# Kernel optimization log

Measured on AMD Instinct MI355X. Metric: run time of the kernel, lower is better.

Reference implementation:

```python
import jax, jax.numpy as jnp
import numpy as np

BN_EPS = 1e-5
NUM_GC_LAYERS = 3
NUM_LAYERS = NUM_GC_LAYERS + 4  # 7
N_NODES = 50000
N_EDGES = 600000
DIM = 128


def setup_inputs() -> dict:
    key = jax.random.key(0)
    ks = jax.random.split(key, 9)
    x = jax.random.normal(ks[0], (N_NODES, DIM), dtype=jnp.float32)
    edge_index = jax.random.randint(ks[1], (2, N_EDGES), 0, N_NODES, dtype=jnp.int64)
    batch = jnp.zeros((N_NODES,), dtype=jnp.int64)
    s = 0.1
    W1 = jax.random.normal(ks[2], (NUM_LAYERS, DIM, DIM), dtype=jnp.float32) * s
    b1 = jax.random.normal(ks[3], (NUM_LAYERS, DIM), dtype=jnp.float32) * s
    W2 = jax.random.normal(ks[4], (NUM_LAYERS, DIM, DIM), dtype=jnp.float32) * s
    b2 = jax.random.normal(ks[5], (NUM_LAYERS, DIM), dtype=jnp.float32) * s
    gamma = jnp.ones((NUM_LAYERS, DIM), dtype=jnp.float32)
    beta = jnp.zeros((NUM_LAYERS, DIM), dtype=jnp.float32)
    return {"x": x, "edge_index": edge_index, "batch": batch,
            "W1": W1, "b1": b1, "W2": W2, "b2": b2,
            "gamma": gamma, "beta": beta}


def _gin_conv(x, src, dst, W1, b1, W2, b2):
    # GINConv with eps=0: out = MLP(x + sum_{j in N(i)} x_j)
    agg = jax.ops.segment_sum(x[src], dst, num_segments=x.shape[0])  # [N, D]
    h = x + agg
    h = jnp.maximum(h @ W1 + b1, 0.0) @ W2 + b2
    return h


def _batch_norm(h, g, b):
    # BatchNorm1d in training mode: biased batch stats over nodes
    mean = jnp.mean(h, axis=0)
    var = jnp.var(h, axis=0)
    return (h - mean) * jax.lax.rsqrt(var + BN_EPS) * g + b


def reference(x, edge_index, batch, W1, b1, W2, b2, gamma, beta):
    src, dst = edge_index[0], edge_index[1]
    for i in range(NUM_GC_LAYERS):
        h = _gin_conv(x, src, dst, W1[i], b1[i], W2[i], b2[i])
        x = _batch_norm(jnp.maximum(h, 0.0), gamma[i], beta[i])
    j = NUM_GC_LAYERS
    outs = []
    for k in range(j, j + 4):
        h = _gin_conv(x, src, dst, W1[k], b1[k], W2[k], b2[k])
        outs.append(_batch_norm(jnp.tanh(h), gamma[k], beta[k]))
    return tuple(outs)
```

## Files before the change

kernel.cpp:

```cpp
#include <hip/hip_runtime.h>
#include <math.h>

#define NN 50000
#define NE 600000
#define DIM 128
#define NLAYERS 7
#define LDK 136
#define BN_EPS 1e-5f
#define GB 782
#define PART_SLOT 200192

typedef __attribute__((ext_vector_type(4))) float floatx4;
typedef __attribute__((ext_vector_type(8))) _Float16 half8;
typedef __attribute__((ext_vector_type(2))) _Float16 half2v;

__device__ __forceinline__ unsigned short f2h(float f) {
  _Float16 h = (_Float16)f;
  return __builtin_bit_cast(unsigned short, h);
}
__device__ __forceinline__ float2 up(unsigned int u) {
  half2v h = __builtin_bit_cast(half2v, u);
  return make_float2((float)h.x, (float)h.y);
}
__device__ __forceinline__ unsigned int pk(float a, float b) {
  half2v h;
  h.x = (_Float16)a;
  h.y = (_Float16)b;
  return __builtin_bit_cast(unsigned int, h);
}


__global__ void hist_kernel(const int* __restrict__ ei, int* __restrict__ deg) {
  int e = blockIdx.x * 256 + threadIdx.x;
  if (e < NE) atomicAdd(&deg[ei[NE + e]], 1);
}

__global__ __launch_bounds__(256) void scan_part(const int* __restrict__ deg,
                                                 int* __restrict__ rowl,
                                                 int* __restrict__ bsum) {
  int b = blockIdx.x, t = threadIdx.x;
  int base = b * 1024 + t * 4;
  int d[4];
  #pragma unroll
  for (int j = 0; j < 4; j++) d[j] = (base + j < NN) ? deg[base + j] : 0;
  int s = d[0] + d[1] + d[2] + d[3];
  int lane = t & 63;
  int incl = s;
  #pragma unroll
  for (int off = 1; off < 64; off <<= 1) {
    int n = __shfl_up(incl, off);
    if (lane >= off) incl += n;
  }
  __shared__ int wtot[4];
  if (lane == 63) wtot[t >> 6] = incl;
  __syncthreads();
  int woff = 0;
  for (int w = 0; w < (t >> 6); w++) woff += wtot[w];
  int run = woff + incl - s;
  #pragma unroll
  for (int j = 0; j < 4; j++) {
    if (base + j < NN) rowl[base + j] = run;
    run += d[j];
  }
  if (t == 255) bsum[b] = woff + incl;
}

__global__ void scan_top(const int* __restrict__ bsum, int* __restrict__ boff,
                         int* __restrict__ row) {
  int t = threadIdx.x;
  int v = (t < 49) ? bsum[t] : 0;
  int incl = v;
  #pragma unroll
  for (int off = 1; off < 64; off <<= 1) {
    int n = __shfl_up(incl, off);
    if (t >= off) incl += n;
  }
  if (t < 49) boff[t] = incl - v;
  if (t == 48) row[NN] = incl;
}

__global__ __launch_bounds__(256) void scan_apply(const int* __restrict__ rowl,
                                                  const int* __restrict__ boff,
                                                  int* __restrict__ row,
                                                  int* __restrict__ cur) {
  int i = blockIdx.x * 256 + threadIdx.x;
  if (i < NN) {
    int r = rowl[i] + boff[i >> 10];
    row[i] = r;
    cur[i] = r;
  }
}

__global__ void bucket_kernel(const int* __restrict__ ei, int* __restrict__ cur,
                              int* __restrict__ esrc) {
  int e = blockIdx.x * 256 + threadIdx.x;
  if (e < NE) {
    int d = ei[NE + e];
    int p = atomicAdd(&cur[d], 1);
    esrc[p] = ei[e];
  }
}


__global__ void convw_kernel(const float* __restrict__ W1, const float* __restrict__ W2,
                             unsigned short* __restrict__ wb) {
  int i = blockIdx.x * 256 + threadIdx.x;
  if (i >= NLAYERS * 16384) return;
  int l = i >> 14;
  int r = i & 16383;
  int n = r >> 7;
  int k = r & 127;
  wb[(size_t)(l * 2 + 0) * 16384 + n * 128 + k] = f2h(W1[(size_t)l * 16384 + k * 128 + n]);
  wb[(size_t)(l * 2 + 1) * 16384 + n * 128 + k] = f2h(W2[(size_t)l * 16384 + k * 128 + n]);
}

__global__ __launch_bounds__(256) void convx_kernel(const float* __restrict__ x,
                                                    unsigned int* __restrict__ x16) {
  int i = blockIdx.x * 256 + threadIdx.x;
  float4 v = ((const float4*)x)[i];
  uint2 o;
  o.x = pk(v.x, v.y);
  o.y = pk(v.z, v.w);
  ((uint2*)x16)[i] = o;
}


__global__ __launch_bounds__(256) void gather_kernel(
    const unsigned int* __restrict__ x16, const int* __restrict__ esrc,
    const int* __restrict__ row, unsigned int* __restrict__ agg16) {
  int w = (blockIdx.x * 256 + threadIdx.x) >> 6;
  int lane = threadIdx.x & 63;
  if (w >= NN) return;
  int s0 = row[w], s1 = row[w + 1];
  float ax = 0.f, ay = 0.f;
  int e = s0;
  for (; e + 3 < s1; e += 4) {
    int i0 = esrc[e], i1 = esrc[e + 1], i2 = esrc[e + 2], i3 = esrc[e + 3];
    unsigned int v0 = x16[i0 * 64 + lane];
    unsigned int v1 = x16[i1 * 64 + lane];
    unsigned int v2 = x16[i2 * 64 + lane];
    unsigned int v3 = x16[i3 * 64 + lane];
    float2 f0 = up(v0), f1 = up(v1), f2 = up(v2), f3 = up(v3);
    ax += (f0.x + f1.x) + (f2.x + f3.x);
    ay += (f0.y + f1.y) + (f2.y + f3.y);
  }
  for (; e < s1; e++) {
    float2 f = up(x16[esrc[e] * 64 + lane]);
    ax += f.x;
    ay += f.y;
  }
  agg16[w * 64 + lane] = pk(ax, ay);
}


__global__ __launch_bounds__(256) void mlp1_kernel(
    const unsigned int* __restrict__ x16, const unsigned int* __restrict__ agg16,
    const unsigned short* __restrict__ wb,
    const float* __restrict__ b1, const float* __restrict__ b2,
    unsigned short* __restrict__ xout16, float* __restrict__ part,
    const float* __restrict__ bnPrev, const float* __restrict__ gPrev,
    const float* __restrict__ btPrev, const int* __restrict__ deg, int hasPrev) {
  __shared__ unsigned short hS[64 * LDK];
  __shared__ unsigned short wS[128 * LDK];
  __shared__ float scshS[256];
  int tid = threadIdx.x;
  int row0 = blockIdx.x * 64;

  if (tid < 128) {
    float sc = 1.f, sh = 0.f;
    if (hasPrev) {
      const float inv = 1.f / (float)NN;
      float mean = bnPrev[tid] * inv;
      float var = bnPrev[128 + tid] * inv - mean * mean;
      sc = gPrev[tid] * rsqrtf(var + BN_EPS);
      sh = btPrev[tid] - mean * sc;
    }
    scshS[tid] = sc;
    scshS[128 + tid] = sh;
  }
  __syncthreads();

  for (int idx = tid; idx < 1024; idx += 256) {
    int r = idx >> 4;
    int c = (idx & 15) * 8;
    uint4 hv = {0u, 0u, 0u, 0u};
    if (row0 + r < NN) {
      size_t base = (size_t)(row0 + r) * 16 + (c >> 3);
      uint4 xv = ((const uint4*)x16)[base];
      uint4 av = ((const uint4*)agg16)[base];
      float dr = 1.f + (float)deg[row0 + r];
      unsigned int xs[4] = {xv.x, xv.y, xv.z, xv.w};
      unsigned int as_[4] = {av.x, av.y, av.z, av.w};
      unsigned int hs[4];
      #pragma unroll
      for (int j = 0; j < 4; j++) {
        float2 xf = up(xs[j]);
        float2 af = up(as_[j]);
        int cc = c + j * 2;
        float h0 = scshS[cc] * (xf.x + af.x) + dr * scshS[128 + cc];
        float h1 = scshS[cc + 1] * (xf.y + af.y) + dr * scshS[128 + cc + 1];
        hs[j] = pk(h0, h1);
      }
      hv.x = hs[0]; hv.y = hs[1]; hv.z = hs[2]; hv.w = hs[3];
    }
    *(uint4*)&hS[r * LDK + c] = hv;
  }
  for (int q = tid; q < 2048; q += 256) {
    int rw = q >> 4;
    int c8 = (q & 15) * 8;
    *(uint4*)&wS[rw * LDK + c8] = *(const uint4*)(wb + rw * 128 + c8);
  }
  __syncthreads();

  int lane = tid & 63;
  int wav = tid >> 6;
  int quad = lane >> 4;
  int lm = lane & 15;
  int mrow = wav * 16 + lm;

  floatx4 acc[8];
  #pragma unroll
  for (int nt = 0; nt < 8; nt++) {
    floatx4 c = {0.f, 0.f, 0.f, 0.f};
    #pragma unroll
    for (int ks = 0; ks < 4; ks++) {
      half8 af = *(half8*)&hS[mrow * LDK + ks * 32 + quad * 8];
      half8 bf = *(half8*)&wS[(nt * 16 + lm) * LDK + ks * 32 + quad * 8];
      c = __builtin_amdgcn_mfma_f32_16x16x32_f16(af, bf, c, 0, 0, 0);
    }
    acc[nt] = c;
  }
  #pragma unroll
  for (int nt = 0; nt < 8; nt++) {
    float bv = b1[nt * 16 + lm];
    #pragma unroll
    for (int rg = 0; rg < 4; rg++) {
      float v = acc[nt][rg] + bv;
      v = v > 0.f ? v : 0.f;
      hS[(wav * 16 + quad * 4 + rg) * LDK + nt * 16 + lm] = f2h(v);
    }
  }
  __syncthreads();
  for (int q = tid; q < 2048; q += 256) {
    int rw = q >> 4;
    int c8 = (q & 15) * 8;
    *(uint4*)&wS[rw * LDK + c8] = *(const uint4*)(wb + 16384 + rw * 128 + c8);
  }
  __syncthreads();

  bool wvalid = (row0 + wav * 16) < NN;
  float sArr[8], sqArr[8];
  #pragma unroll
  for (int nt = 0; nt < 8; nt++) {
    floatx4 c = {0.f, 0.f, 0.f, 0.f};
    #pragma unroll
    for (int ks = 0; ks < 4; ks++) {
      half8 af = *(half8*)&hS[mrow * LDK + ks * 32 + quad * 8];
      half8 bf = *(half8*)&wS[(nt * 16 + lm) * LDK + ks * 32 + quad * 8];
      c = __builtin_amdgcn_mfma_f32_16x16x32_f16(af, bf, c, 0, 0, 0);
    }
    float bv = b2[nt * 16 + lm];
    float s = 0.f, sq = 0.f;
    #pragma unroll
    for (int rg = 0; rg < 4; rg++) {
      float v = c[rg] + bv;
      v = v > 0.f ? v : 0.f;
      if (wvalid)
        xout16[(size_t)(row0 + wav * 16 + quad * 4 + rg) * DIM + nt * 16 + lm] = f2h(v);
      s += v;
      sq += v * v;
    }
    s += __shfl_xor(s, 16);
    s += __shfl_xor(s, 32);
    sq += __shfl_xor(sq, 16);
    sq += __shfl_xor(sq, 32);
    sArr[nt] = s;
    sqArr[nt] = sq;
  }
  __syncthreads();
  float* redS = (float*)hS;
  if (quad == 0) {
    #pragma unroll
    for (int nt = 0; nt < 8; nt++) {
      redS[wav * 256 + nt * 16 + lm] = wvalid ? sArr[nt] : 0.f;
      redS[wav * 256 + 128 + nt * 16 + lm] = wvalid ? sqArr[nt] : 0.f;
    }
  }
  __syncthreads();
  float v = redS[tid] + redS[256 + tid] + redS[512 + tid] + redS[768 + tid];
  part[(size_t)blockIdx.x * 256 + tid] = v;
}


__global__ __launch_bounds__(256) void mlp4_kernel(
    const unsigned int* __restrict__ x16, const unsigned int* __restrict__ agg16,
    const unsigned short* __restrict__ wbg,
    const float* __restrict__ b1g, const float* __restrict__ b2g,
    float* __restrict__ out, float* __restrict__ partBase,
    const float* __restrict__ bnPrev, const float* __restrict__ gPrev,
    const float* __restrict__ btPrev, const int* __restrict__ deg) {
  __shared__ unsigned short hS[64 * LDK];
  __shared__ unsigned short wS[128 * LDK];
  __shared__ float scshS[256];
  int tid = threadIdx.x;
  int row0 = blockIdx.x * 64;

  if (tid < 128) {
    const float inv = 1.f / (float)NN;
    float mean = bnPrev[tid] * inv;
    float var = bnPrev[128 + tid] * inv - mean * mean;
    float sc = gPrev[tid] * rsqrtf(var + BN_EPS);
    scshS[tid] = sc;
    scshS[128 + tid] = btPrev[tid] - mean * sc;
  }
  __syncthreads();

  for (int idx = tid; idx < 1024; idx += 256) {
    int r = idx >> 4;
    int c = (idx & 15) * 8;
    uint4 hv = {0u, 0u, 0u, 0u};
    if (row0 + r < NN) {
      size_t base = (size_t)(row0 + r) * 16 + (c >> 3);
      uint4 xv = ((const uint4*)x16)[base];
      uint4 av = ((const uint4*)agg16)[base];
      float dr = 1.f + (float)deg[row0 + r];
      unsigned int xs[4] = {xv.x, xv.y, xv.z, xv.w};
      unsigned int as_[4] = {av.x, av.y, av.z, av.w};
      unsigned int hs[4];
      #pragma unroll
      for (int j = 0; j < 4; j++) {
        float2 xf = up(xs[j]);
        float2 af = up(as_[j]);
        int cc = c + j * 2;
        float h0 = scshS[cc] * (xf.x + af.x) + dr * scshS[128 + cc];
        float h1 = scshS[cc + 1] * (xf.y + af.y) + dr * scshS[128 + cc + 1];
        hs[j] = pk(h0, h1);
      }
      hv.x = hs[0]; hv.y = hs[1]; hv.z = hs[2]; hv.w = hs[3];
    }
    *(uint4*)&hS[r * LDK + c] = hv;
  }
  __syncthreads();

  int lane = tid & 63;
  int wav = tid >> 6;
  int quad = lane >> 4;
  int lm = lane & 15;
  int mrow = wav * 16 + lm;
  bool wvalid = (row0 + wav * 16) < NN;

  half8 aF[4];
  #pragma unroll
  for (int ks = 0; ks < 4; ks++)
    aF[ks] = *(half8*)&hS[mrow * LDK + ks * 32 + quad * 8];

  #pragma unroll 1
  for (int ly = 0; ly < 4; ly++) {
    int layer = 3 + ly;
    const unsigned short* wb = wbg + (size_t)layer * 2 * 16384;
    const float* b1 = b1g + layer * 128;
    const float* b2 = b2g + layer * 128;
    float* act = out + (size_t)ly * NN * DIM;
    float* part = partBase + (size_t)ly * PART_SLOT;

    __syncthreads();
    for (int q = tid; q < 2048; q += 256) {
      int rw = q >> 4;
      int c8 = (q & 15) * 8;
      *(uint4*)&wS[rw * LDK + c8] = *(const uint4*)(wb + rw * 128 + c8);
    }
    __syncthreads();

    floatx4 acc[8];
    #pragma unroll
    for (int nt = 0; nt < 8; nt++) {
      floatx4 c = {0.f, 0.f, 0.f, 0.f};
      #pragma unroll
      for (int ks = 0; ks < 4; ks++) {
        half8 bf = *(half8*)&wS[(nt * 16 + lm) * LDK + ks * 32 + quad * 8];
        c = __builtin_amdgcn_mfma_f32_16x16x32_f16(aF[ks], bf, c, 0, 0, 0);
      }
      acc[nt] = c;
    }
    #pragma unroll
    for (int nt = 0; nt < 8; nt++) {
      float bv = b1[nt * 16 + lm];
      #pragma unroll
      for (int rg = 0; rg < 4; rg++) {
        float v = acc[nt][rg] + bv;
        v = v > 0.f ? v : 0.f;
        hS[(wav * 16 + quad * 4 + rg) * LDK + nt * 16 + lm] = f2h(v);
      }
    }
    __syncthreads();
    for (int q = tid; q < 2048; q += 256) {
      int rw = q >> 4;
      int c8 = (q & 15) * 8;
      *(uint4*)&wS[rw * LDK + c8] = *(const uint4*)(wb + 16384 + rw * 128 + c8);
    }
    __syncthreads();

    float sArr[8], sqArr[8];
    #pragma unroll
    for (int nt = 0; nt < 8; nt++) {
      floatx4 c = {0.f, 0.f, 0.f, 0.f};
      #pragma unroll
      for (int ks = 0; ks < 4; ks++) {
        half8 af = *(half8*)&hS[mrow * LDK + ks * 32 + quad * 8];
        half8 bf = *(half8*)&wS[(nt * 16 + lm) * LDK + ks * 32 + quad * 8];
        c = __builtin_amdgcn_mfma_f32_16x16x32_f16(af, bf, c, 0, 0, 0);
      }
      float bv = b2[nt * 16 + lm];
      float s = 0.f, sq = 0.f;
      #pragma unroll
      for (int rg = 0; rg < 4; rg++) {
        float v = c[rg] + bv;
        v = tanhf(v);
        if (wvalid)
          act[(size_t)(row0 + wav * 16 + quad * 4 + rg) * DIM + nt * 16 + lm] = v;
        s += v;
        sq += v * v;
      }
      s += __shfl_xor(s, 16);
      s += __shfl_xor(s, 32);
      sq += __shfl_xor(sq, 16);
      sq += __shfl_xor(sq, 32);
      sArr[nt] = s;
      sqArr[nt] = sq;
    }
    __syncthreads();
    float* redS = (float*)hS;
    if (quad == 0) {
      #pragma unroll
      for (int nt = 0; nt < 8; nt++) {
        redS[wav * 256 + nt * 16 + lm] = wvalid ? sArr[nt] : 0.f;
        redS[wav * 256 + 128 + nt * 16 + lm] = wvalid ? sqArr[nt] : 0.f;
      }
    }
    __syncthreads();
    float v = redS[tid] + redS[256 + tid] + redS[512 + tid] + redS[768 + tid];
    part[(size_t)blockIdx.x * 256 + tid] = v;
  }
}


__global__ __launch_bounds__(256) void reduce_kernel(const float* __restrict__ part,
                                                     float* __restrict__ bn) {
  int c = blockIdx.x;
  int t = threadIdx.x;
  const float* p = part + (size_t)blockIdx.y * PART_SLOT + c;
  float s = 0.f;
  for (int b = t; b < GB; b += 256) s += p[(size_t)b * 256];
  #pragma unroll
  for (int off = 1; off < 64; off <<= 1) s += __shfl_xor(s, off);
  __shared__ float wsum[4];
  if ((t & 63) == 0) wsum[t >> 6] = s;
  __syncthreads();
  if (t == 0) bn[blockIdx.y * 256 + c] = wsum[0] + wsum[1] + wsum[2] + wsum[3];
}


__global__ __launch_bounds__(256) void norm_kernel(
    const float* __restrict__ aBase, const float* __restrict__ bnAll,
    const float* __restrict__ gammaAll, const float* __restrict__ betaAll,
    float* __restrict__ oBase, int layer0) {
  int layer = layer0 + blockIdx.y;
  const float* a = aBase + (size_t)blockIdx.y * NN * DIM;
  const float* bn = bnAll + blockIdx.y * 256;
  const float* gamma = gammaAll + layer * 128;
  const float* beta = betaAll + layer * 128;
  float* o = oBase + (size_t)blockIdx.y * NN * DIM;
  int i = blockIdx.x * 256 + threadIdx.x;
  int f = (i & 31) * 4;
  const float inv = 1.f / (float)NN;
  float4 v = ((const float4*)a)[i];
  float r[4] = {v.x, v.y, v.z, v.w};
  #pragma unroll
  for (int j = 0; j < 4; j++) {
    float mean = bn[f + j] * inv;
    float var = bn[128 + f + j] * inv - mean * mean;
    float sc = gamma[f + j] * rsqrtf(var + BN_EPS);
    r[j] = (r[j] - mean) * sc + beta[f + j];
  }
  float4 ov; ov.x = r[0]; ov.y = r[1]; ov.z = r[2]; ov.w = r[3];
  ((float4*)o)[i] = ov;
}


extern "C" void kernel_launch(void* const* d_in, const int* in_sizes, int n_in,
                              void* d_out, int out_size, void* d_ws, size_t ws_size,
                              hipStream_t stream) {
  const float* x_in = (const float*)d_in[0];
  const int* ei = (const int*)d_in[1];
  const float* W1g = (const float*)d_in[3];
  const float* b1g = (const float*)d_in[4];
  const float* W2g = (const float*)d_in[5];
  const float* b2g = (const float*)d_in[6];
  const float* gg = (const float*)d_in[7];
  const float* bg = (const float*)d_in[8];
  float* out = (float*)d_out;

  char* ws = (char*)d_ws;
  const size_t OFF_X16 = 0;
  const size_t OFF_A16 = 12800000;
  const size_t OFF_WB = 25600000;
  const size_t OFF_BN = 26058752;
  const size_t OFF_DEG = 26062848;
  const size_t OFF_ROW = 26262848;
  const size_t OFF_CUR = 26462852;
  const size_t OFF_ESR = 26662852;
  const size_t OFF_PART = 29062852;

  unsigned int* X16 = (unsigned int*)(ws + OFF_X16);
  unsigned int* A16 = (unsigned int*)(ws + OFF_A16);
  unsigned short* wb = (unsigned short*)(ws + OFF_WB);
  float* bn = (float*)(ws + OFF_BN);
  int* deg = (int*)(ws + OFF_DEG);
  int* rowp = (int*)(ws + OFF_ROW);
  int* cur = (int*)(ws + OFF_CUR);
  int* esrc = (int*)(ws + OFF_ESR);
  float* part = (float*)(ws + OFF_PART);
  int* rowl = (int*)(ws + OFF_PART);
  int* bsum = (int*)(ws + OFF_PART + 800000);
  int* boff = (int*)(ws + OFF_PART + 800256);

  hipMemsetAsync(deg, 0, NN * sizeof(int), stream);
  hist_kernel<<<(NE + 255) / 256, 256, 0, stream>>>(ei, deg);
  scan_part<<<49, 256, 0, stream>>>(deg, rowl, bsum);
  scan_top<<<1, 64, 0, stream>>>(bsum, boff, rowp);
  scan_apply<<<196, 256, 0, stream>>>(rowl, boff, rowp, cur);
  bucket_kernel<<<(NE + 255) / 256, 256, 0, stream>>>(ei, cur, esrc);
  convw_kernel<<<(NLAYERS * 16384 + 255) / 256, 256, 0, stream>>>(W1g, W2g, wb);
  convx_kernel<<<NN * DIM / 4 / 256, 256, 0, stream>>>(x_in, X16);

  for (int i = 0; i < 3; i++) {
    gather_kernel<<<(NN * 64 + 255) / 256, 256, 0, stream>>>(X16, esrc, rowp, A16);
    mlp1_kernel<<<GB, 256, 0, stream>>>(
        X16, A16, wb + (size_t)i * 2 * 16384, b1g + i * 128, b2g + i * 128,
        (unsigned short*)X16, part,
        (i == 0) ? bn : bn + (i - 1) * 256,
        (i == 0) ? gg : gg + (i - 1) * 128,
        (i == 0) ? bg : bg + (i - 1) * 128, deg, i > 0 ? 1 : 0);
    reduce_kernel<<<dim3(256, 1), 256, 0, stream>>>(part, bn + i * 256);
  }
  gather_kernel<<<(NN * 64 + 255) / 256, 256, 0, stream>>>(X16, esrc, rowp, A16);
  mlp4_kernel<<<GB, 256, 0, stream>>>(X16, A16, wb, b1g, b2g, out, part,
                                      bn + 2 * 256, gg + 2 * 128, bg + 2 * 128, deg);
  reduce_kernel<<<dim3(256, 4), 256, 0, stream>>>(part, bn);
  norm_kernel<<<dim3(NN * DIM / 4 / 256, 4), 256, 0, stream>>>(out, bn, gg, bg, out, 3);
}
```

Measured before the change: 519.1 us.

## Halve MLP shared memory with XOR swizzle and register-prefetched weight halves

The MLP kernels drop the padded LDS layout for an XOR-swizzled 128-wide one and stage weights in 64-row halves, so each block uses about half the shared memory and launch bounds request four blocks per CU. The next weight half is prefetched into registers while MFMAs run on the current one, and biases are folded into the accumulator init. The tanh layers use an exp/rcp fast tanh, and the gather loop is unrolled by eight to keep more loads in flight. The cost is extra barriers per layer, more register pressure, and slightly less accurate tanh.

```diff
diff --git a/kernel.cpp b/kernel.cpp
--- a/kernel.cpp
+++ b/kernel.cpp
@@ -5,7 +5,6 @@
 #define NE 600000
 #define DIM 128
 #define NLAYERS 7
-#define LDK 136
 #define BN_EPS 1e-5f
 #define GB 782
 #define PART_SLOT 200192
@@ -27,6 +26,13 @@
   h.x = (_Float16)a;
   h.y = (_Float16)b;
   return __builtin_bit_cast(unsigned int, h);
+}
+__device__ __forceinline__ float tanh_fast(float x) {
+  float e = __expf(2.0f * x);
+  return 1.0f - 2.0f * __builtin_amdgcn_rcpf(e + 1.0f);
+}
+__device__ __forceinline__ int hsw(int row, int scol) {
+  return row * 128 + (scol ^ ((row & 7) << 3));
 }
 
 
@@ -134,6 +140,20 @@
   int s0 = row[w], s1 = row[w + 1];
   float ax = 0.f, ay = 0.f;
   int e = s0;
+  for (; e + 7 < s1; e += 8) {
+    int idx[8];
+    #pragma unroll
+    for (int j = 0; j < 8; j++) idx[j] = esrc[e + j];
+    unsigned int v[8];
+    #pragma unroll
+    for (int j = 0; j < 8; j++) v[j] = x16[idx[j] * 64 + lane];
+    #pragma unroll
+    for (int j = 0; j < 8; j++) {
+      float2 f = up(v[j]);
+      ax += f.x;
+      ay += f.y;
+    }
+  }
   for (; e + 3 < s1; e += 4) {
     int i0 = esrc[e], i1 = esrc[e + 1], i2 = esrc[e + 2], i3 = esrc[e + 3];
     unsigned int v0 = x16[i0 * 64 + lane];
@@ -153,15 +173,15 @@
 }
 
 
-__global__ __launch_bounds__(256) void mlp1_kernel(
+__global__ __launch_bounds__(256, 4) void mlp1_kernel(
     const unsigned int* __restrict__ x16, const unsigned int* __restrict__ agg16,
     const unsigned short* __restrict__ wb,
     const float* __restrict__ b1, const float* __restrict__ b2,
     unsigned short* __restrict__ xout16, float* __restrict__ part,
     const float* __restrict__ bnPrev, const float* __restrict__ gPrev,
     const float* __restrict__ btPrev, const int* __restrict__ deg, int hasPrev) {
-  __shared__ unsigned short hS[64 * LDK];
-  __shared__ unsigned short wS[128 * LDK];
+  __shared__ unsigned short hS[64 * 128];
+  __shared__ unsigned short wS[64 * 128];
   __shared__ float scshS[256];
   int tid = threadIdx.x;
   int row0 = blockIdx.x * 64;
@@ -178,37 +198,41 @@
     scshS[tid] = sc;
     scshS[128 + tid] = sh;
   }
-  __syncthreads();
-
-  for (int idx = tid; idx < 1024; idx += 256) {
+
+  uint4 wreg[4];
+  #pragma unroll
+  for (int j = 0; j < 4; j++) {
+    int q = tid + j * 256;
+    wreg[j] = *(const uint4*)(wb + (q >> 4) * 128 + (q & 15) * 8);
+  }
+  __syncthreads();
+
+  #pragma unroll
+  for (int j = 0; j < 4; j++) {
+    int idx = tid + j * 256;
     int r = idx >> 4;
     int c = (idx & 15) * 8;
     uint4 hv = {0u, 0u, 0u, 0u};
     if (row0 + r < NN) {
-      size_t base = (size_t)(row0 + r) * 16 + (c >> 3);
+      size_t base = (size_t)(row0 + r) * 16 + (idx & 15);
       uint4 xv = ((const uint4*)x16)[base];
       uint4 av = ((const uint4*)agg16)[base];
       float dr = 1.f + (float)deg[row0 + r];
       unsigned int xs[4] = {xv.x, xv.y, xv.z, xv.w};
       unsigned int as_[4] = {av.x, av.y, av.z, av.w};
-      unsigned int hs[4];
-      #pragma unroll
-      for (int j = 0; j < 4; j++) {
-        float2 xf = up(xs[j]);
-        float2 af = up(as_[j]);
-        int cc = c + j * 2;
+      unsigned int hs4[4];
+      #pragma unroll
+      for (int jj = 0; jj < 4; jj++) {
+        float2 xf = up(xs[jj]);
+        float2 af = up(as_[jj]);
+        int cc = c + jj * 2;
         float h0 = scshS[cc] * (xf.x + af.x) + dr * scshS[128 + cc];
         float h1 = scshS[cc + 1] * (xf.y + af.y) + dr * scshS[128 + cc + 1];
-        hs[j] = pk(h0, h1);
-      }
-      hv.x = hs[0]; hv.y = hs[1]; hv.z = hs[2]; hv.w = hs[3];
-    }
-    *(uint4*)&hS[r * LDK + c] = hv;
-  }
-  for (int q = tid; q < 2048; q += 256) {
-    int rw = q >> 4;
-    int c8 = (q & 15) * 8;
-    *(uint4*)&wS[rw * LDK + c8] = *(const uint4*)(wb + rw * 128 + c8);
+        hs4[jj] = pk(h0, h1);
+      }
+      hv.x = hs4[0]; hv.y = hs4[1]; hv.z = hs4[2]; hv.w = hs4[3];
+    }
+    *(uint4*)&hS[hsw(r, c)] = hv;
   }
   __syncthreads();
 
@@ -217,53 +241,122 @@
   int quad = lane >> 4;
   int lm = lane & 15;
   int mrow = wav * 16 + lm;
+  bool wvalid = (row0 + wav * 16) < NN;
+
+  half8 aF[4];
+  #pragma unroll
+  for (int ks = 0; ks < 4; ks++)
+    aF[ks] = *(half8*)&hS[hsw(mrow, ks * 32 + quad * 8)];
+
+  #pragma unroll
+  for (int j = 0; j < 4; j++) {
+    int q = tid + j * 256;
+    *(uint4*)&wS[hsw(q >> 4, (q & 15) * 8)] = wreg[j];
+  }
+  #pragma unroll
+  for (int j = 0; j < 4; j++) {
+    int q = tid + j * 256;
+    wreg[j] = *(const uint4*)(wb + 8192 + (q >> 4) * 128 + (q & 15) * 8);
+  }
+  __syncthreads();
 
   floatx4 acc[8];
   #pragma unroll
+  for (int nt = 0; nt < 4; nt++) {
+    float bv = b1[nt * 16 + lm];
+    floatx4 cacc = {bv, bv, bv, bv};
+    #pragma unroll
+    for (int ks = 0; ks < 4; ks++) {
+      half8 bf = *(half8*)&wS[hsw(nt * 16 + lm, ks * 32 + quad * 8)];
+      cacc = __builtin_amdgcn_mfma_f32_16x16x32_f16(aF[ks], bf, cacc, 0, 0, 0);
+    }
+    acc[nt] = cacc;
+  }
+  __syncthreads();
+  #pragma unroll
+  for (int j = 0; j < 4; j++) {
+    int q = tid + j * 256;
+    *(uint4*)&wS[hsw(q >> 4, (q & 15) * 8)] = wreg[j];
+  }
+  #pragma unroll
+  for (int j = 0; j < 4; j++) {
+    int q = tid + j * 256;
+    wreg[j] = *(const uint4*)(wb + 16384 + (q >> 4) * 128 + (q & 15) * 8);
+  }
+  __syncthreads();
+  #pragma unroll
+  for (int nt = 4; nt < 8; nt++) {
+    float bv = b1[nt * 16 + lm];
+    floatx4 cacc = {bv, bv, bv, bv};
+    #pragma unroll
+    for (int ks = 0; ks < 4; ks++) {
+      half8 bf = *(half8*)&wS[hsw((nt - 4) * 16 + lm, ks * 32 + quad * 8)];
+      cacc = __builtin_amdgcn_mfma_f32_16x16x32_f16(aF[ks], bf, cacc, 0, 0, 0);
+    }
+    acc[nt] = cacc;
+  }
+  #pragma unroll
   for (int nt = 0; nt < 8; nt++) {
-    floatx4 c = {0.f, 0.f, 0.f, 0.f};
+    #pragma unroll
+    for (int rg = 0; rg < 4; rg++) {
+      float v = acc[nt][rg];
+      v = v > 0.f ? v : 0.f;
+      hS[hsw(wav * 16 + quad * 4 + rg, nt * 16 + lm)] = f2h(v);
+    }
+  }
+  __syncthreads();
+  #pragma unroll
+  for (int j = 0; j < 4; j++) {
+    int q = tid + j * 256;
+    *(uint4*)&wS[hsw(q >> 4, (q & 15) * 8)] = wreg[j];
+  }
+  #pragma unroll
+  for (int j = 0; j < 4; j++) {
+    int q = tid + j * 256;
+    wreg[j] = *(const uint4*)(wb + 24576 + (q >> 4) * 128 + (q & 15) * 8);
+  }
+  __syncthreads();
+  half8 aG[4];
+  #pragma unroll
+  for (int ks = 0; ks < 4; ks++)
+    aG[ks] = *(half8*)&hS[hsw(mrow, ks * 32 + quad * 8)];
+  #pragma unroll
+  for (int nt = 0; nt < 4; nt++) {
+    float bv = b2[nt * 16 + lm];
+    floatx4 cacc = {bv, bv, bv, bv};
     #pragma unroll
     for (int ks = 0; ks < 4; ks++) {
-      half8 af = *(half8*)&hS[mrow * LDK + ks * 32 + quad * 8];
-      half8 bf = *(half8*)&wS[(nt * 16 + lm) * LDK + ks * 32 + quad * 8];
-      c = __builtin_amdgcn_mfma_f32_16x16x32_f16(af, bf, c, 0, 0, 0);
-    }
-    acc[nt] = c;
-  }
+      half8 bf = *(half8*)&wS[hsw(nt * 16 + lm, ks * 32 + quad * 8)];
+      cacc = __builtin_amdgcn_mfma_f32_16x16x32_f16(aG[ks], bf, cacc, 0, 0, 0);
+    }
+    acc[nt] = cacc;
+  }
+  __syncthreads();
+  #pragma unroll
+  for (int j = 0; j < 4; j++) {
+    int q = tid + j * 256;
+    *(uint4*)&wS[hsw(q >> 4, (q & 15) * 8)] = wreg[j];
+  }
+  __syncthreads();
+  #pragma unroll
+  for (int nt = 4; nt < 8; nt++) {
+    float bv = b2[nt * 16 + lm];
+    floatx4 cacc = {bv, bv, bv, bv};
+    #pragma unroll
+    for (int ks = 0; ks < 4; ks++) {
+      half8 bf = *(half8*)&wS[hsw((nt - 4) * 16 + lm, ks * 32 + quad * 8)];
+      cacc = __builtin_amdgcn_mfma_f32_16x16x32_f16(aG[ks], bf, cacc, 0, 0, 0);
+    }
+    acc[nt] = cacc;
+  }
+
+  float sArr[8], sqArr[8];
   #pragma unroll
   for (int nt = 0; nt < 8; nt++) {
-    float bv = b1[nt * 16 + lm];
+    float s = 0.f, sq = 0.f;
     #pragma unroll
     for (int rg = 0; rg < 4; rg++) {
-      float v = acc[nt][rg] + bv;
-      v = v > 0.f ? v : 0.f;
-      hS[(wav * 16 + quad * 4 + rg) * LDK + nt * 16 + lm] = f2h(v);
-    }
-  }
-  __syncthreads();
-  for (int q = tid; q < 2048; q += 256) {
-    int rw = q >> 4;
-    int c8 = (q & 15) * 8;
-    *(uint4*)&wS[rw * LDK + c8] = *(const uint4*)(wb + 16384 + rw * 128 + c8);
-  }
-  __syncthreads();
-
-  bool wvalid = (row0 + wav * 16) < NN;
-  float sArr[8], sqArr[8];
-  #pragma unroll
-  for (int nt = 0; nt < 8; nt++) {
-    floatx4 c = {0.f, 0.f, 0.f, 0.f};
-    #pragma unroll
-    for (int ks = 0; ks < 4; ks++) {
-      half8 af = *(half8*)&hS[mrow * LDK + ks * 32 + quad * 8];
-      half8 bf = *(half8*)&wS[(nt * 16 + lm) * LDK + ks * 32 + quad * 8];
-      c = __builtin_amdgcn_mfma_f32_16x16x32_f16(af, bf, c, 0, 0, 0);
-    }
-    float bv = b2[nt * 16 + lm];
-    float s = 0.f, sq = 0.f;
-    #pragma unroll
-    for (int rg = 0; rg < 4; rg++) {
-      float v = c[rg] + bv;
+      float v = acc[nt][rg];
       v = v > 0.f ? v : 0.f;
       if (wvalid)
         xout16[(size_t)(row0 + wav * 16 + quad * 4 + rg) * DIM + nt * 16 + lm] = f2h(v);
@@ -292,15 +385,15 @@
 }
 
 
-__global__ __launch_bounds__(256) void mlp4_kernel(
+__global__ __launch_bounds__(256, 4) void mlp4f_kernel(
     const unsigned int* __restrict__ x16, const unsigned int* __restrict__ agg16,
     const unsigned short* __restrict__ wbg,
     const float* __restrict__ b1g, const float* __restrict__ b2g,
     float* __restrict__ out, float* __restrict__ partBase,
     const float* __restrict__ bnPrev, const float* __restrict__ gPrev,
     const float* __restrict__ btPrev, const int* __restrict__ deg) {
-  __shared__ unsigned short hS[64 * LDK];
-  __shared__ unsigned short wS[128 * LDK];
+  __shared__ unsigned short hS[64 * 128];
+  __shared__ unsigned short wS[64 * 128];
   __shared__ float scshS[256];
   int tid = threadIdx.x;
   int row0 = blockIdx.x * 64;
@@ -313,32 +406,41 @@
     scshS[tid] = sc;
     scshS[128 + tid] = btPrev[tid] - mean * sc;
   }
-  __syncthreads();
-
-  for (int idx = tid; idx < 1024; idx += 256) {
+
+  uint4 wreg[4];
+  #pragma unroll
+  for (int j = 0; j < 4; j++) {
+    int q = tid + j * 256;
+    wreg[j] = *(const uint4*)(wbg + (q >> 4) * 128 + (q & 15) * 8);
+  }
+  __syncthreads();
+
+  #pragma unroll
+  for (int j = 0; j < 4; j++) {
+    int idx = tid + j * 256;
     int r = idx >> 4;
     int c = (idx & 15) * 8;
     uint4 hv = {0u, 0u, 0u, 0u};
     if (row0 + r < NN) {
-      size_t base = (size_t)(row0 + r) * 16 + (c >> 3);
+      size_t base = (size_t)(row0 + r) * 16 + (idx & 15);
       uint4 xv = ((const uint4*)x16)[base];
       uint4 av = ((const uint4*)agg16)[base];
       float dr = 1.f + (float)deg[row0 + r];
       unsigned int xs[4] = {xv.x, xv.y, xv.z, xv.w};
       unsigned int as_[4] = {av.x, av.y, av.z, av.w};
-      unsigned int hs[4];
-      #pragma unroll
-      for (int j = 0; j < 4; j++) {
-        float2 xf = up(xs[j]);
-        float2 af = up(as_[j]);
-        int cc = c + j * 2;
+      unsigned int hs4[4];
+      #pragma unroll
+      for (int jj = 0; jj < 4; jj++) {
+        float2 xf = up(xs[jj]);
+        float2 af = up(as_[jj]);
+        int cc = c + jj * 2;
         float h0 = scshS[cc] * (xf.x + af.x) + dr * scshS[128 + cc];
         float h1 = scshS[cc + 1] * (xf.y + af.y) + dr * scshS[128 + cc + 1];
-        hs[j] = pk(h0, h1);
-      }
-      hv.x = hs[0]; hv.y = hs[1]; hv.z = hs[2]; hv.w = hs[3];
-    }
-    *(uint4*)&hS[r * LDK + c] = hv;
+        hs4[jj] = pk(h0, h1);
+      }
+      hv.x = hs4[0]; hv.y = hs4[1]; hv.z = hs4[2]; hv.w = hs4[3];
+    }
+    *(uint4*)&hS[hsw(r, c)] = hv;
   }
   __syncthreads();
 
@@ -352,70 +454,137 @@
   half8 aF[4];
   #pragma unroll
   for (int ks = 0; ks < 4; ks++)
-    aF[ks] = *(half8*)&hS[mrow * LDK + ks * 32 + quad * 8];
+    aF[ks] = *(half8*)&hS[hsw(mrow, ks * 32 + quad * 8)];
 
   #pragma unroll 1
   for (int ly = 0; ly < 4; ly++) {
-    int layer = 3 + ly;
-    const unsigned short* wb = wbg + (size_t)layer * 2 * 16384;
-    const float* b1 = b1g + layer * 128;
-    const float* b2 = b2g + layer * 128;
+    const unsigned short* wb = wbg + (size_t)ly * 32768;
+    const float* b1 = b1g + ly * 128;
+    const float* b2 = b2g + ly * 128;
     float* act = out + (size_t)ly * NN * DIM;
     float* part = partBase + (size_t)ly * PART_SLOT;
 
-    __syncthreads();
-    for (int q = tid; q < 2048; q += 256) {
-      int rw = q >> 4;
-      int c8 = (q & 15) * 8;
-      *(uint4*)&wS[rw * LDK + c8] = *(const uint4*)(wb + rw * 128 + c8);
+    #pragma unroll
+    for (int j = 0; j < 4; j++) {
+      int q = tid + j * 256;
+      *(uint4*)&wS[hsw(q >> 4, (q & 15) * 8)] = wreg[j];
+    }
+    #pragma unroll
+    for (int j = 0; j < 4; j++) {
+      int q = tid + j * 256;
+      wreg[j] = *(const uint4*)(wb + 8192 + (q >> 4) * 128 + (q & 15) * 8);
     }
     __syncthreads();
 
     floatx4 acc[8];
     #pragma unroll
+    for (int nt = 0; nt < 4; nt++) {
+      float bv = b1[nt * 16 + lm];
+      floatx4 cacc = {bv, bv, bv, bv};
+      #pragma unroll
+      for (int ks = 0; ks < 4; ks++) {
+        half8 bf = *(half8*)&wS[hsw(nt * 16 + lm, ks * 32 + quad * 8)];
+        cacc = __builtin_amdgcn_mfma_f32_16x16x32_f16(aF[ks], bf, cacc, 0, 0, 0);
+      }
+      acc[nt] = cacc;
+    }
+    __syncthreads();
+
+    #pragma unroll
+    for (int j = 0; j < 4; j++) {
+      int q = tid + j * 256;
+      *(uint4*)&wS[hsw(q >> 4, (q & 15) * 8)] = wreg[j];
+    }
+    #pragma unroll
+    for (int j = 0; j < 4; j++) {
+      int q = tid + j * 256;
+      wreg[j] = *(const uint4*)(wb + 16384 + (q >> 4) * 128 + (q & 15) * 8);
+    }
+    __syncthreads();
+    #pragma unroll
+    for (int nt = 4; nt < 8; nt++) {
+      float bv = b1[nt * 16 + lm];
+      floatx4 cacc = {bv, bv, bv, bv};
+      #pragma unroll
+      for (int ks = 0; ks < 4; ks++) {
+        half8 bf = *(half8*)&wS[hsw((nt - 4) * 16 + lm, ks * 32 + quad * 8)];
+        cacc = __builtin_amdgcn_mfma_f32_16x16x32_f16(aF[ks], bf, cacc, 0, 0, 0);
+      }
+      acc[nt] = cacc;
+    }
+    #pragma unroll
     for (int nt = 0; nt < 8; nt++) {
-      floatx4 c = {0.f, 0.f, 0.f, 0.f};
+      #pragma unroll
+      for (int rg = 0; rg < 4; rg++) {
+        float v = acc[nt][rg];
+        v = v > 0.f ? v : 0.f;
+        hS[hsw(wav * 16 + quad * 4 + rg, nt * 16 + lm)] = f2h(v);
+      }
+    }
+    __syncthreads();
+
+    #pragma unroll
+    for (int j = 0; j < 4; j++) {
+      int q = tid + j * 256;
+      *(uint4*)&wS[hsw(q >> 4, (q & 15) * 8)] = wreg[j];
+    }
+    #pragma unroll
+    for (int j = 0; j < 4; j++) {
+      int q = tid + j * 256;
+      wreg[j] = *(const uint4*)(wb + 24576 + (q >> 4) * 128 + (q & 15) * 8);
+    }
+    __syncthreads();
+    half8 aG[4];
+    #pragma unroll
+    for (int ks = 0; ks < 4; ks++)
+      aG[ks] = *(half8*)&hS[hsw(mrow, ks * 32 + quad * 8)];
+    #pragma unroll
+    for (int nt = 0; nt < 4; nt++) {
+      float bv = b2[nt * 16 + lm];
+      floatx4 cacc = {bv, bv, bv, bv};
       #pragma unroll
       for (int ks = 0; ks < 4; ks++) {
-        half8 bf = *(half8*)&wS[(nt * 16 + lm) * LDK + ks * 32 + quad * 8];
-        c = __builtin_amdgcn_mfma_f32_16x16x32_f16(aF[ks], bf, c, 0, 0, 0);
-      }
-      acc[nt] = c;
-    }
+        half8 bf = *(half8*)&wS[hsw(nt * 16 + lm, ks * 32 + quad * 8)];
+        cacc = __builtin_amdgcn_mfma_f32_16x16x32_f16(aG[ks], bf, cacc, 0, 0, 0);
+      }
+      acc[nt] = cacc;
+    }
+    __syncthreads();
+
+    #pragma unroll
+    for (int j = 0; j < 4; j++) {
+      int q = tid + j * 256;
+      *(uint4*)&wS[hsw(q >> 4, (q & 15) * 8)] = wreg[j];
+    }
+    {
+      size_t nxt = (ly < 3) ? (size_t)(ly + 1) * 32768 : 0;
+      #pragma unroll
+      for (int j = 0; j < 4; j++) {
+        int q = tid + j * 256;
+        wreg[j] = *(const uint4*)(wbg + nxt + (q >> 4) * 128 + (q & 15) * 8);
+      }
+    }
+    __syncthreads();
+    #pragma unroll
+    for (int nt = 4; nt < 8; nt++) {
+      float bv = b2[nt * 16 + lm];
+      floatx4 cacc = {bv, bv, bv, bv};
+      #pragma unroll
+      for (int ks = 0; ks < 4; ks++) {
+        half8 bf = *(half8*)&wS[hsw((nt - 4) * 16 + lm, ks * 32 + quad * 8)];
+        cacc = __builtin_amdgcn_mfma_f32_16x16x32_f16(aG[ks], bf, cacc, 0, 0, 0);
+      }
+      acc[nt] = cacc;
+    }
+
+    float sArr[8], sqArr[8];
     #pragma unroll
     for (int nt = 0; nt < 8; nt++) {
-      float bv = b1[nt * 16 + lm];
+      float s = 0.f, sq = 0.f;
       #pragma unroll
       for (int rg = 0; rg < 4; rg++) {
-        float v = acc[nt][rg] + bv;
-        v = v > 0.f ? v : 0.f;
-        hS[(wav * 16 + quad * 4 + rg) * LDK + nt * 16 + lm] = f2h(v);
-      }
-    }
-    __syncthreads();
-    for (int q = tid; q < 2048; q += 256) {
-      int rw = q >> 4;
-      int c8 = (q & 15) * 8;
-      *(uint4*)&wS[rw * LDK + c8] = *(const uint4*)(wb + 16384 + rw * 128 + c8);
-    }
-    __syncthreads();
-
-    float sArr[8], sqArr[8];
-    #pragma unroll
-    for (int nt = 0; nt < 8; nt++) {
-      floatx4 c = {0.f, 0.f, 0.f, 0.f};
-      #pragma unroll
-      for (int ks = 0; ks < 4; ks++) {
-        half8 af = *(half8*)&hS[mrow * LDK + ks * 32 + quad * 8];
-        half8 bf = *(half8*)&wS[(nt * 16 + lm) * LDK + ks * 32 + quad * 8];
-        c = __builtin_amdgcn_mfma_f32_16x16x32_f16(af, bf, c, 0, 0, 0);
-      }
-      float bv = b2[nt * 16 + lm];
-      float s = 0.f, sq = 0.f;
-      #pragma unroll
-      for (int rg = 0; rg < 4; rg++) {
-        float v = c[rg] + bv;
-        v = tanhf(v);
+        float v = acc[nt][rg];
+        v = tanh_fast(v);
         if (wvalid)
           act[(size_t)(row0 + wav * 16 + quad * 4 + rg) * DIM + nt * 16 + lm] = v;
         s += v;
@@ -536,7 +705,7 @@
   for (int i = 0; i < 3; i++) {
     gather_kernel<<<(NN * 64 + 255) / 256, 256, 0, stream>>>(X16, esrc, rowp, A16);
     mlp1_kernel<<<GB, 256, 0, stream>>>(
-        X16, A16, wb + (size_t)i * 2 * 16384, b1g + i * 128, b2g + i * 128,
+        X16, A16, wb + (size_t)i * 32768, b1g + i * 128, b2g + i * 128,
         (unsigned short*)X16, part,
         (i == 0) ? bn : bn + (i - 1) * 256,
         (i == 0) ? gg : gg + (i - 1) * 128,
@@ -544,8 +713,9 @@
     reduce_kernel<<<dim3(256, 1), 256, 0, stream>>>(part, bn + i * 256);
   }
   gather_kernel<<<(NN * 64 + 255) / 256, 256, 0, stream>>>(X16, esrc, rowp, A16);
-  mlp4_kernel<<<GB, 256, 0, stream>>>(X16, A16, wb, b1g, b2g, out, part,
-                                      bn + 2 * 256, gg + 2 * 128, bg + 2 * 128, deg);
+  mlp4f_kernel<<<GB, 256, 0, stream>>>(X16, A16, wb + 3 * 32768, b1g + 3 * 128,
+                                       b2g + 3 * 128, out, part,
+                                       bn + 2 * 256, gg + 2 * 128, bg + 2 * 128, deg);
   reduce_kernel<<<dim3(256, 4), 256, 0, stream>>>(part, bn);
   norm_kernel<<<dim3(NN * DIM / 4 / 256, 4), 256, 0, stream>>>(out, bn, gg, bg, out, 3);
 }
```

New measurement: 556.8 us. +7.3%, slower.
